# Kernel optimization log

Hardware: AMD Instinct MI355X
Metric: run time of the kernel (lower is better)

## Reference

```python
import jax, jax.numpy as jnp
import numpy as np

EPS = 0.0  # init eps


def setup_inputs() -> dict:
    key = jax.random.key(0)
    k1, k2 = jax.random.split(key)
    features = jax.random.normal(k1, (8, 64, 100000), dtype=jnp.float32)
    coords = jax.random.normal(k2, (8, 3, 100000), dtype=jnp.float32)
    return {"features": features, "coords": coords, "resolution": 32}


def _voxelize(features, coords, r):
    # coords: [B, 3, N], features: [B, C, N]
    coords = jax.lax.stop_gradient(coords)  # original does coords.detach()
    norm_coords = coords - jnp.mean(coords, axis=2, keepdims=True)
    # normalize=True branch: divide by 2*max point radius, shift to [0,1]
    radius = jnp.linalg.norm(norm_coords, axis=1, keepdims=True)        # [B,1,N]
    scale = jnp.max(radius, axis=2, keepdims=True) * 2.0 + EPS          # [B,1,1]
    norm_coords = norm_coords / scale + 0.5
    norm_coords = jnp.clip(norm_coords * r, 0, r - 1)                   # [B,3,N]
    vox = jnp.round(norm_coords).astype(jnp.int32)                      # [B,3,N]

    B, C, N = features.shape
    flat_idx = (vox[:, 0] * r + vox[:, 1]) * r + vox[:, 2]              # [B,N]
    seg_ids = (flat_idx + jnp.arange(B, dtype=jnp.int32)[:, None] * (r ** 3)).reshape(-1)

    feats = jnp.transpose(features, (0, 2, 1)).reshape(B * N, C)        # [B*N,C]
    sums = jax.ops.segment_sum(feats, seg_ids, num_segments=B * r ** 3)  # [B*r^3,C]
    cnts = jax.ops.segment_sum(jnp.ones((B * N,), features.dtype), seg_ids,
                               num_segments=B * r ** 3)                  # [B*r^3]
    avg = sums / jnp.maximum(cnts, 1.0)[:, None]
    vox_feat = jnp.transpose(avg.reshape(B, r ** 3, C), (0, 2, 1)).reshape(B, C, r, r, r)
    return vox_feat, norm_coords


def reference(features, coords, resolution):
    return _voxelize(features, coords, int(resolution))
```

## Files before the change

kernel.cpp:

```cpp
#include <hip/hip_runtime.h>
#include <math.h>

static constexpr int B = 8;
static constexpr int C = 64;
static constexpr int N = 100000;
static constexpr int RES = 32;
static constexpr int R3 = RES * RES * RES;

static constexpr int   SCALE_BITS = 19;
static constexpr float FSCALE     = (float)(1 << SCALE_BITS);
static constexpr float INV_FSCALE = 1.0f / FSCALE;

static constexpr size_t MEAN_OFF = 0;
static constexpr size_t MAX_OFF  = 192;
static constexpr size_t CNT_OFF  = 256;
static constexpr size_t VID_OFF  = CNT_OFF + (size_t)B * R3 * sizeof(int);
static constexpr size_t HDR_BYTES = 256;

__device__ __forceinline__ int vhash(int v) { return v ^ (v >> 5) ^ (v >> 10); }

__device__ __forceinline__ double block_reduce_sum(double v) {
    for (int off = 32; off > 0; off >>= 1) v += __shfl_down(v, off, 64);
    __shared__ double s[4];
    int lane = threadIdx.x & 63, w = threadIdx.x >> 6;
    if (lane == 0) s[w] = v;
    __syncthreads();
    if (threadIdx.x == 0) v = (s[0] + s[1]) + (s[2] + s[3]);
    return v;
}

__device__ __forceinline__ float block_reduce_max(float v) {
    for (int off = 32; off > 0; off >>= 1) v = fmaxf(v, __shfl_down(v, off, 64));
    __shared__ float s[4];
    int lane = threadIdx.x & 63, w = threadIdx.x >> 6;
    if (lane == 0) s[w] = v;
    __syncthreads();
    if (threadIdx.x == 0) v = fmaxf(fmaxf(s[0], s[1]), fmaxf(s[2], s[3]));
    return v;
}

__global__ void k_mean(const float* __restrict__ coords, double* __restrict__ mean_sum,
                       int* __restrict__ cnt) {
    int gtid = blockIdx.x * blockDim.x + threadIdx.x;
    int4* c4 = (int4*)cnt;
    for (int i = gtid; i < B * R3 / 4; i += gridDim.x * blockDim.x)
        c4[i] = make_int4(0, 0, 0, 0);

    const int NSLICE = 8;
    int pair  = blockIdx.x % (B * 3);
    int slice = blockIdx.x / (B * 3);
    const float* p = coords + (size_t)pair * N;
    double acc = 0.0;
#pragma unroll 4
    for (int i = slice * 256 + threadIdx.x; i < N; i += NSLICE * 256)
        acc += (double)p[i];
    acc = block_reduce_sum(acc);
    if (threadIdx.x == 0) atomicAdd(&mean_sum[pair], acc);
}

__global__ void k_max(const float* __restrict__ coords,
                      const double* __restrict__ mean_sum,
                      unsigned int* __restrict__ maxr2) {
    const int NSLICE = 16;
    int b     = blockIdx.x % B;
    int slice = blockIdx.x / B;
    float mx = (float)(mean_sum[b * 3 + 0] / (double)N);
    float my = (float)(mean_sum[b * 3 + 1] / (double)N);
    float mz = (float)(mean_sum[b * 3 + 2] / (double)N);
    const float* px = coords + (size_t)(b * 3 + 0) * N;
    const float* py = coords + (size_t)(b * 3 + 1) * N;
    const float* pz = coords + (size_t)(b * 3 + 2) * N;
    float m = 0.0f;
#pragma unroll 4
    for (int i = slice * 256 + threadIdx.x; i < N; i += NSLICE * 256) {
        float x = px[i] - mx, y = py[i] - my, z = pz[i] - mz;
        m = fmaxf(m, x * x + y * y + z * z);
    }
    m = block_reduce_max(m);
    if (threadIdx.x == 0) atomicMax(&maxr2[b], __float_as_uint(m));
}

__global__ void k_vid(const float* __restrict__ coords,
                      const double* __restrict__ mean_sum,
                      const unsigned int* __restrict__ maxr2,
                      unsigned short* __restrict__ vid,
                      float* __restrict__ out_norm,
                      int* __restrict__ cnt) {
    int idx = blockIdx.x * blockDim.x + threadIdx.x;
    if (idx >= B * N) return;
    int b = idx / N;
    int n = idx - b * N;
    float scale = 2.0f * sqrtf(__uint_as_float(maxr2[b]));
    int iv[3];
#pragma unroll
    for (int d = 0; d < 3; ++d) {
        float mean = (float)(mean_sum[b * 3 + d] / (double)N);
        float p = coords[(size_t)(b * 3 + d) * N + n];
        float v = (p - mean) / scale + 0.5f;
        v = v * (float)RES;
        v = fminf(fmaxf(v, 0.0f), (float)(RES - 1));
        out_norm[(size_t)(b * 3 + d) * N + n] = v;
        iv[d] = (int)rintf(v);
    }
    int flat = (iv[0] * RES + iv[1]) * RES + iv[2];
    vid[idx] = (unsigned short)flat;
    atomicAdd(&cnt[b * R3 + flat], 1);
}

__global__ __launch_bounds__(1024) void k_accum(const unsigned short* __restrict__ vid,
                                                const float* __restrict__ feats,
                                                const int* __restrict__ cnt,
                                                float* __restrict__ out_vox) {
    extern __shared__ char smem[];
    int* grid = (int*)smem;
    constexpr int BS = 1024, U = 4, STEP = BS * U;
    constexpr int NQ = N / 4;
    constexpr int NITER = NQ / STEP;
    constexpr int NMAIN = NITER * STEP;
    int b = blockIdx.x & 7;
    int c = blockIdx.x >> 3;
    int4* g4 = (int4*)grid;
    for (int i = threadIdx.x; i < R3 / 4; i += BS) g4[i] = make_int4(0, 0, 0, 0);
    __syncthreads();
    const uint2*  vp = (const uint2*)(vid + (size_t)b * N);
    const float4* fp = (const float4*)(feats + ((size_t)(b * C + c)) * N);
    const int tid = threadIdx.x;

    uint2 v0[U], v1[U]; float4 f0[U], f1[U];

#define LOADC(dstv, dstf, chunk)                                            \
    {   int _base = (chunk) * STEP + tid;                                   \
        _Pragma("unroll")                                                   \
        for (int u = 0; u < U; ++u) { dstv[u] = vp[_base + u * BS];         \
                                      dstf[u] = fp[_base + u * BS]; } }
#define PROC(sv, sf)                                                        \
    {   _Pragma("unroll")                                                   \
        for (int u = 0; u < U; ++u) {                                       \
            uint2 vv = sv[u]; float4 ff = sf[u];                            \
            atomicAdd(&grid[vhash((int)(vv.x & 0xffffu))], __float2int_rn(ff.x * FSCALE)); \
            atomicAdd(&grid[vhash((int)(vv.x >> 16))],     __float2int_rn(ff.y * FSCALE)); \
            atomicAdd(&grid[vhash((int)(vv.y & 0xffffu))], __float2int_rn(ff.z * FSCALE)); \
            atomicAdd(&grid[vhash((int)(vv.y >> 16))],     __float2int_rn(ff.w * FSCALE)); \
        } }

    LOADC(v0, f0, 0);
    for (int it = 0; it < NITER; it += 2) {
        int c1 = (it + 1 < NITER) ? it + 1 : NITER - 1;
        LOADC(v1, f1, c1);
        __builtin_amdgcn_sched_barrier(0);
        PROC(v0, f0);
        int c2 = (it + 2 < NITER) ? it + 2 : NITER - 1;
        LOADC(v0, f0, c2);
        __builtin_amdgcn_sched_barrier(0);
        PROC(v1, f1);
    }
#undef LOADC
#undef PROC
    for (int i = NMAIN + tid; i < NQ; i += BS) {
        uint2 v = vp[i]; float4 f = fp[i];
        atomicAdd(&grid[vhash((int)(v.x & 0xffffu))], __float2int_rn(f.x * FSCALE));
        atomicAdd(&grid[vhash((int)(v.x >> 16))],     __float2int_rn(f.y * FSCALE));
        atomicAdd(&grid[vhash((int)(v.y & 0xffffu))], __float2int_rn(f.z * FSCALE));
        atomicAdd(&grid[vhash((int)(v.y >> 16))],     __float2int_rn(f.w * FSCALE));
    }
    __syncthreads();
    const int* cp = cnt + (size_t)b * R3;
    float* op = out_vox + ((size_t)(b * C + c)) * R3;
    for (int i = threadIdx.x; i < R3; i += BS) {
        float s = (float)grid[vhash(i)] * INV_FSCALE;
        op[i] = s / fmaxf((float)cp[i], 1.0f);
    }
}

extern "C" void kernel_launch(void* const* d_in, const int* in_sizes, int n_in,
                              void* d_out, int out_size, void* d_ws, size_t ws_size,
                              hipStream_t stream) {
    const float* feats  = (const float*)d_in[0];
    const float* coords = (const float*)d_in[1];
    float* out_vox  = (float*)d_out;
    float* out_norm = out_vox + (size_t)B * C * R3;

    double*         mean_sum = (double*)((char*)d_ws + MEAN_OFF);
    unsigned int*   maxr2    = (unsigned int*)((char*)d_ws + MAX_OFF);
    int*            cnt      = (int*)((char*)d_ws + CNT_OFF);
    unsigned short* vid      = (unsigned short*)((char*)d_ws + VID_OFF);

    static bool attr_done = false;
    if (!attr_done) {
        hipFuncSetAttribute((const void*)k_accum,
                            hipFuncAttributeMaxDynamicSharedMemorySize, R3 * sizeof(int));
        attr_done = true;
    }

    hipMemsetAsync(d_ws, 0, HDR_BYTES, stream);

    k_mean<<<B * 3 * 8, 256, 0, stream>>>(coords, mean_sum, cnt);
    k_max<<<B * 16, 256, 0, stream>>>(coords, mean_sum, maxr2);
    k_vid<<<(B * N + 255) / 256, 256, 0, stream>>>(coords, mean_sum, maxr2, vid, out_norm, cnt);
    k_accum<<<B * C, 1024, R3 * sizeof(int), stream>>>(vid, feats, cnt, out_vox);
}
```

Measured before the change: 385.8 us.

## Fuse all voxelization stages into one cooperative kernel with grid syncs

Replaces the four separate launches (mean, max radius, voxel id/count, accumulate) with a single cooperative kernel of 256 blocks of 1024 threads, separated by grid-wide syncs. Each block handles two channels in the accumulate phase instead of one block per (batch, channel). This removes launch gaps between stages, but it halves the number of accumulation blocks from 512 to 256 and adds grid-sync cost. It falls back to the old multi-kernel path if the cooperative launch fails.

```diff
diff --git a/kernel.cpp b/kernel.cpp
--- a/kernel.cpp
+++ b/kernel.cpp
@@ -1,5 +1,8 @@
 #include <hip/hip_runtime.h>
+#include <hip/hip_cooperative_groups.h>
 #include <math.h>
+
+namespace cg = cooperative_groups;
 
 static constexpr int B = 8;
 static constexpr int C = 64;
@@ -18,6 +21,184 @@
 static constexpr size_t HDR_BYTES = 256;
 
 __device__ __forceinline__ int vhash(int v) { return v ^ (v >> 5) ^ (v >> 10); }
+
+__device__ __forceinline__ double block_reduce_sum_1k(double v) {
+    for (int off = 32; off > 0; off >>= 1) v += __shfl_down(v, off, 64);
+    __shared__ double s[16];
+    int lane = threadIdx.x & 63, w = threadIdx.x >> 6;
+    if (lane == 0) s[w] = v;
+    __syncthreads();
+    if (threadIdx.x == 0) {
+        double t = 0.0;
+#pragma unroll
+        for (int i = 0; i < 16; ++i) t += s[i];
+        v = t;
+    }
+    __syncthreads();
+    return v;
+}
+
+__device__ __forceinline__ float block_reduce_max_1k(float v) {
+    for (int off = 32; off > 0; off >>= 1) v = fmaxf(v, __shfl_down(v, off, 64));
+    __shared__ float s[16];
+    int lane = threadIdx.x & 63, w = threadIdx.x >> 6;
+    if (lane == 0) s[w] = v;
+    __syncthreads();
+    if (threadIdx.x == 0) {
+        float t = s[0];
+#pragma unroll
+        for (int i = 1; i < 16; ++i) t = fmaxf(t, s[i]);
+        v = t;
+    }
+    __syncthreads();
+    return v;
+}
+
+__global__ __launch_bounds__(1024) void k_fused(
+    const float* __restrict__ coords, const float* __restrict__ feats,
+    double* __restrict__ mean_sum, unsigned int* __restrict__ maxr2,
+    unsigned short* __restrict__ vid, int* __restrict__ cnt,
+    float* __restrict__ out_norm, float* __restrict__ out_vox)
+{
+    cg::grid_group gg = cg::this_grid();
+    extern __shared__ char smem[];
+    int* grid = (int*)smem;
+    const int tid = threadIdx.x;
+    const int bid = blockIdx.x;
+
+    {
+        int gtid = bid * 1024 + tid;
+        if (gtid < B * R3 / 4) ((int4*)cnt)[gtid] = make_int4(0, 0, 0, 0);
+    }
+
+    if (bid < 240) {
+        int pair  = bid % 24;
+        int slice = bid / 24;
+        const float* p = coords + (size_t)pair * N;
+        double acc = 0.0;
+#pragma unroll 4
+        for (int i = slice * 1024 + tid; i < N; i += 10 * 1024)
+            acc += (double)p[i];
+        acc = block_reduce_sum_1k(acc);
+        if (tid == 0) atomicAdd(&mean_sum[pair], acc);
+    }
+    gg.sync();
+
+    {
+        int b     = bid & 7;
+        int slice = bid >> 3;
+        float mx = (float)(mean_sum[b * 3 + 0] / (double)N);
+        float my = (float)(mean_sum[b * 3 + 1] / (double)N);
+        float mz = (float)(mean_sum[b * 3 + 2] / (double)N);
+        const float* px = coords + (size_t)(b * 3 + 0) * N;
+        const float* py = coords + (size_t)(b * 3 + 1) * N;
+        const float* pz = coords + (size_t)(b * 3 + 2) * N;
+        float m = 0.0f;
+#pragma unroll 4
+        for (int i = slice * 1024 + tid; i < N; i += 32 * 1024) {
+            float x = px[i] - mx, y = py[i] - my, z = pz[i] - mz;
+            m = fmaxf(m, x * x + y * y + z * z);
+        }
+        m = block_reduce_max_1k(m);
+        if (tid == 0) atomicMax(&maxr2[b], __float_as_uint(m));
+    }
+    gg.sync();
+
+    {
+        int b   = bid & 7;
+        int seg = bid >> 3;
+        float scale = 2.0f * sqrtf(__uint_as_float(maxr2[b]));
+        float m0 = (float)(mean_sum[b * 3 + 0] / (double)N);
+        float m1 = (float)(mean_sum[b * 3 + 1] / (double)N);
+        float m2 = (float)(mean_sum[b * 3 + 2] / (double)N);
+        const float* p0 = coords + (size_t)(b * 3 + 0) * N;
+        const float* p1 = coords + (size_t)(b * 3 + 1) * N;
+        const float* p2 = coords + (size_t)(b * 3 + 2) * N;
+        float* o0 = out_norm + (size_t)(b * 3 + 0) * N;
+        float* o1 = out_norm + (size_t)(b * 3 + 1) * N;
+        float* o2 = out_norm + (size_t)(b * 3 + 2) * N;
+        unsigned short* vp = vid + (size_t)b * N;
+        int* cb = cnt + (size_t)b * R3;
+        for (int i = seg * 1024 + tid; i < N; i += 32 * 1024) {
+            float v0 = (p0[i] - m0) / scale + 0.5f; v0 = v0 * (float)RES;
+            v0 = fminf(fmaxf(v0, 0.0f), (float)(RES - 1));
+            float v1 = (p1[i] - m1) / scale + 0.5f; v1 = v1 * (float)RES;
+            v1 = fminf(fmaxf(v1, 0.0f), (float)(RES - 1));
+            float v2 = (p2[i] - m2) / scale + 0.5f; v2 = v2 * (float)RES;
+            v2 = fminf(fmaxf(v2, 0.0f), (float)(RES - 1));
+            o0[i] = v0; o1[i] = v1; o2[i] = v2;
+            int iv0 = (int)rintf(v0), iv1 = (int)rintf(v1), iv2 = (int)rintf(v2);
+            int flat = (iv0 * RES + iv1) * RES + iv2;
+            vp[i] = (unsigned short)flat;
+            atomicAdd(&cb[flat], 1);
+        }
+    }
+    gg.sync();
+
+    {
+        int b  = bid & 7;
+        int c0 = bid >> 3;
+        constexpr int BS = 1024, U = 4, STEP = BS * U;
+        constexpr int NQ = N / 4;
+        constexpr int NITER = NQ / STEP;
+        constexpr int NMAIN = NITER * STEP;
+        const int* cp = cnt + (size_t)b * R3;
+
+        for (int rep = 0; rep < 2; ++rep) {
+            int c = c0 + rep * 32;
+            __syncthreads();
+            int4* g4 = (int4*)grid;
+            for (int i = tid; i < R3 / 4; i += BS) g4[i] = make_int4(0, 0, 0, 0);
+            __syncthreads();
+
+            const uint2*  vp = (const uint2*)(vid + (size_t)b * N);
+            const float4* fp = (const float4*)(feats + ((size_t)(b * C + c)) * N);
+            uint2 v0[U], v1[U]; float4 f0[U], f1[U];
+
+#define LOADC(dstv, dstf, chunk)                                            \
+    {   int _base = (chunk) * STEP + tid;                                   \
+        _Pragma("unroll")                                                   \
+        for (int u = 0; u < U; ++u) { dstv[u] = vp[_base + u * BS];         \
+                                      dstf[u] = fp[_base + u * BS]; } }
+#define PROC(sv, sf)                                                        \
+    {   _Pragma("unroll")                                                   \
+        for (int u = 0; u < U; ++u) {                                       \
+            uint2 vv = sv[u]; float4 ff = sf[u];                            \
+            atomicAdd(&grid[vhash((int)(vv.x & 0xffffu))], __float2int_rn(ff.x * FSCALE)); \
+            atomicAdd(&grid[vhash((int)(vv.x >> 16))],     __float2int_rn(ff.y * FSCALE)); \
+            atomicAdd(&grid[vhash((int)(vv.y & 0xffffu))], __float2int_rn(ff.z * FSCALE)); \
+            atomicAdd(&grid[vhash((int)(vv.y >> 16))],     __float2int_rn(ff.w * FSCALE)); \
+        } }
+
+            LOADC(v0, f0, 0);
+            for (int it = 0; it < NITER; it += 2) {
+                int c1 = (it + 1 < NITER) ? it + 1 : NITER - 1;
+                LOADC(v1, f1, c1);
+                __builtin_amdgcn_sched_barrier(0);
+                PROC(v0, f0);
+                int c2 = (it + 2 < NITER) ? it + 2 : NITER - 1;
+                LOADC(v0, f0, c2);
+                __builtin_amdgcn_sched_barrier(0);
+                PROC(v1, f1);
+            }
+            for (int i = NMAIN + tid; i < NQ; i += BS) {
+                uint2 v = vp[i]; float4 f = fp[i];
+                atomicAdd(&grid[vhash((int)(v.x & 0xffffu))], __float2int_rn(f.x * FSCALE));
+                atomicAdd(&grid[vhash((int)(v.x >> 16))],     __float2int_rn(f.y * FSCALE));
+                atomicAdd(&grid[vhash((int)(v.y & 0xffffu))], __float2int_rn(f.z * FSCALE));
+                atomicAdd(&grid[vhash((int)(v.y >> 16))],     __float2int_rn(f.w * FSCALE));
+            }
+#undef LOADC
+#undef PROC
+            __syncthreads();
+            float* op = out_vox + ((size_t)(b * C + c)) * R3;
+            for (int i = tid; i < R3; i += BS) {
+                float s = (float)grid[vhash(i)] * INV_FSCALE;
+                op[i] = s / fmaxf((float)cp[i], 1.0f);
+            }
+        }
+    }
+}
 
 __device__ __forceinline__ double block_reduce_sum(double v) {
     for (int off = 32; off > 0; off >>= 1) v += __shfl_down(v, off, 64);
@@ -45,7 +226,6 @@
     int4* c4 = (int4*)cnt;
     for (int i = gtid; i < B * R3 / 4; i += gridDim.x * blockDim.x)
         c4[i] = make_int4(0, 0, 0, 0);
-
     const int NSLICE = 8;
     int pair  = blockIdx.x % (B * 3);
     int slice = blockIdx.x / (B * 3);
@@ -125,9 +305,7 @@
     const uint2*  vp = (const uint2*)(vid + (size_t)b * N);
     const float4* fp = (const float4*)(feats + ((size_t)(b * C + c)) * N);
     const int tid = threadIdx.x;
-
     uint2 v0[U], v1[U]; float4 f0[U], f1[U];
-
 #define LOADC(dstv, dstf, chunk)                                            \
     {   int _base = (chunk) * STEP + tid;                                   \
         _Pragma("unroll")                                                   \
@@ -142,7 +320,6 @@
             atomicAdd(&grid[vhash((int)(vv.y & 0xffffu))], __float2int_rn(ff.z * FSCALE)); \
             atomicAdd(&grid[vhash((int)(vv.y >> 16))],     __float2int_rn(ff.w * FSCALE)); \
         } }
-
     LOADC(v0, f0, 0);
     for (int it = 0; it < NITER; it += 2) {
         int c1 = (it + 1 < NITER) ? it + 1 : NITER - 1;
@@ -185,14 +362,27 @@
     int*            cnt      = (int*)((char*)d_ws + CNT_OFF);
     unsigned short* vid      = (unsigned short*)((char*)d_ws + VID_OFF);
 
-    static bool attr_done = false;
-    if (!attr_done) {
+    static int use_coop = -1;
+    if (use_coop == -1) {
+        hipFuncSetAttribute((const void*)k_fused,
+                            hipFuncAttributeMaxDynamicSharedMemorySize, R3 * sizeof(int));
         hipFuncSetAttribute((const void*)k_accum,
                             hipFuncAttributeMaxDynamicSharedMemorySize, R3 * sizeof(int));
-        attr_done = true;
     }
 
     hipMemsetAsync(d_ws, 0, HDR_BYTES, stream);
+
+    if (use_coop != 0) {
+        void* kargs[] = { (void*)&coords, (void*)&feats, (void*)&mean_sum,
+                          (void*)&maxr2, (void*)&vid, (void*)&cnt,
+                          (void*)&out_norm, (void*)&out_vox };
+        hipError_t e = hipLaunchCooperativeKernel((const void*)k_fused,
+                                                  dim3(256), dim3(1024), kargs,
+                                                  (unsigned)(R3 * sizeof(int)), stream);
+        if (use_coop == -1) use_coop = (e == hipSuccess) ? 1 : 0;
+        if (e == hipSuccess) return;
+        (void)hipGetLastError();
+    }
 
     k_mean<<<B * 3 * 8, 256, 0, stream>>>(coords, mean_sum, cnt);
     k_max<<<B * 16, 256, 0, stream>>>(coords, mean_sum, maxr2);
```

Result: slower. 522.0 us (+35.3%).
